# Kernel tuning notes

Measured on AMD Instinct MI355X. Metric: run time of the kernel, lower is better.

The kernel has to match this reference:

```python
import jax, jax.numpy as jnp
import numpy as np

W_BITS = 8       # default precision = max(precisions)
MIN_PREC = 4     # min(precisions)
GROUP_SIZE = 128


def make_new_byte_indices(total_bytes: int) -> np.ndarray:
    # Replicates make_new_byte_indices_torch. Note: in the torch code,
    # argsort(argsort(new_idx)) == new_idx (it is a permutation), so the
    # "unpermute" is a gather with new_idx itself.
    bytes_per_thread = 4
    threads_per_warp = 32
    bytes_per_warp = threads_per_warp * bytes_per_thread  # 128
    full = total_bytes // bytes_per_warp * bytes_per_warp
    rem = total_bytes - full
    parts = []
    if full > 0:
        bi = np.arange(full)
        warp_offsets = (bi // bytes_per_warp) * bytes_per_warp
        thread_indices = bi % threads_per_warp
        byte_off = ((bi % bytes_per_warp) // threads_per_warp) ^ 3
        parts.append(warp_offsets + thread_indices * bytes_per_thread + byte_off)
    if rem > 0:
        ri = np.arange(rem)
        adj = rem // bytes_per_thread
        if adj > 0:
            warp_offsets = (ri // bytes_per_warp) * bytes_per_warp
            thread_indices = ri % adj
            byte_off = (ri // adj) ^ 3
            parts.append(warp_offsets + thread_indices * 4 + byte_off + full)
        else:
            parts.append(np.arange(full, full + rem))
    return np.concatenate(parts).astype(np.int64)


def dequant(qweight, scale, zero, w_bits=W_BITS):
    _, N, in_chunks = qweight.shape
    total_bytes = in_chunks * 4
    in_features = in_chunks * 32
    q = qweight[:w_bits]
    # little-endian byte view of int32 (matches torch .view(torch.uint8))
    b = jnp.stack([(q >> (8 * k)) & 0xFF for k in range(4)], axis=-1)
    b = b.reshape(w_bits, N, total_bytes)  # int32 values in [0,255]
    idx = jnp.asarray(make_new_byte_indices(total_bytes))
    b = b[:, :, idx]
    # unpack bits, MSB first within each byte
    bits = jnp.stack([(b >> i) & 1 for i in reversed(range(8))], axis=-1)
    bits = bits.reshape(w_bits, N, in_features)  # [w_bits, N, in_features]
    plane_w = jnp.asarray([1 << (w_bits - 1 - k) for k in range(w_bits)], dtype=jnp.int32)
    qw = jnp.einsum('b,bni->ni', plane_w, bits)  # int32 in [0, 2^w_bits-1]
    weight_f = qw.astype(jnp.float32)
    bit_err = w_bits - MIN_PREC
    zero = zero * (2.0 ** bit_err)
    scale_pc = jnp.repeat(scale, GROUP_SIZE, axis=1)[:, :in_features]
    zero_pc = jnp.repeat(zero, GROUP_SIZE, axis=1)[:, :in_features]
    return scale_pc * (weight_f - zero_pc)  # [N, in_features]


def setup_inputs() -> dict:
    key = jax.random.key(0)
    kx, kq, ks, kz, kb = jax.random.split(key, 5)
    B, S, IN, OUT, G = 4, 2048, 4096, 4096, GROUP_SIZE
    x = jax.random.normal(kx, (B, S, IN), dtype=jnp.float32)
    qweight = jax.random.randint(kq, (8, OUT, IN // 32), 0, 2147483647, dtype=jnp.int32)
    scale = jax.random.uniform(ks, (OUT, IN // G), dtype=jnp.float32) * 0.01 + 1e-4
    zero = jax.random.uniform(kz, (OUT, IN // G), dtype=jnp.float32) * 8.0
    bias = jax.random.normal(kb, (OUT,), dtype=jnp.float32)
    return {"x": x, "qweight": qweight, "scale": scale, "zero": zero, "bias": bias}


def reference(x, qweight, scale, zero, bias):
    weight = dequant(qweight, scale, zero, W_BITS)  # [out, in]
    return jnp.matmul(x, weight.T) + bias
```

## Files before the change

### kernel.cpp

```cpp
#include <hip/hip_runtime.h>
#include <hip/hip_bf16.h>
#include <stdint.h>

typedef __attribute__((ext_vector_type(8))) short short8;
typedef __attribute__((ext_vector_type(4))) float f32x4;

#define M_DIM 8192
#define N_DIM 4096
#define K_DIM 4096
#define BM 256
#define BN 256
#define BK 64

static __device__ __forceinline__ unsigned short f32_to_bf16(float f) {
  union { float f; unsigned int u; } v; v.f = f;
  unsigned int u = v.u;
  u += 0x7fffu + ((u >> 16) & 1u);
  return (unsigned short)(u >> 16);
}

__global__ void prep_kernel(const float* __restrict__ x,
                            unsigned short* __restrict__ xb,
                            const int* __restrict__ qw,
                            const float* __restrict__ scale,
                            const float* __restrict__ zero,
                            unsigned short* __restrict__ W) {
  if (blockIdx.x < 16384) {
    size_t i = ((size_t)blockIdx.x * blockDim.x + threadIdx.x) * 8;
    float4 v0 = *reinterpret_cast<const float4*>(x + i);
    float4 v1 = *reinterpret_cast<const float4*>(x + i + 4);
    short8 o;
    o[0] = (short)f32_to_bf16(v0.x);
    o[1] = (short)f32_to_bf16(v0.y);
    o[2] = (short)f32_to_bf16(v0.z);
    o[3] = (short)f32_to_bf16(v0.w);
    o[4] = (short)f32_to_bf16(v1.x);
    o[5] = (short)f32_to_bf16(v1.y);
    o[6] = (short)f32_to_bf16(v1.z);
    o[7] = (short)f32_to_bf16(v1.w);
    *reinterpret_cast<short8*>(xb + i) = o;
  } else {
    int idx = (blockIdx.x - 16384) * blockDim.x + threadIdx.x;
    int n = idx >> 7;
    int c = idx & 127;
    unsigned int w[8];
#pragma unroll
    for (int k = 0; k < 8; ++k)
      w[k] = (unsigned int)qw[(size_t)k * (N_DIM * 128) + idx];
    int wp = c >> 5, t = c & 31;
#pragma unroll
    for (int s = 0; s < 4; ++s) {
      int r = s ^ 3;
      unsigned int by[8];
#pragma unroll
      for (int k = 0; k < 8; ++k) by[k] = (w[k] >> (8 * r)) & 0xffu;
      int ibase = wp * 1024 + s * 256 + t * 8;
      int g = ibase >> 7;
      float sc = scale[n * 32 + g];
      float zp = zero[n * 32 + g] * 16.0f;
      short8 o;
#pragma unroll
      for (int u = 0; u < 8; ++u) {
        unsigned int q = 0;
#pragma unroll
        for (int k = 0; k < 8; ++k)
          q |= ((by[k] >> (7 - u)) & 1u) << (7 - k);
        o[u] = (short)f32_to_bf16(sc * ((float)q - zp));
      }
      *reinterpret_cast<short8*>(&W[(size_t)n * K_DIM + ibase]) = o;
    }
  }
}


#define VMCNT2 asm volatile("s_waitcnt vmcnt(2)" ::: "memory")
#define VMCNT0 asm volatile("s_waitcnt vmcnt(0)" ::: "memory")
#define NOOP ((void)0)
#define SB0 __builtin_amdgcn_sched_barrier(0)

#define STG(G, GROWB, KT, LDSC) do {                                           \
  const unsigned short* sb_ = (G) + ((size_t)(GROWB) * K_DIM + (KT) * 64);     \
  __builtin_amdgcn_global_load_lds(                                            \
      (const __attribute__((address_space(1))) void*)(sb_ + s_off0),           \
      (__attribute__((address_space(3))) void*)(smem + (LDSC) + wslot),        \
      16, 0, 0);                                                               \
  __builtin_amdgcn_global_load_lds(                                            \
      (const __attribute__((address_space(1))) void*)(sb_ + s_off1),           \
      (__attribute__((address_space(3))) void*)(smem + (LDSC) + 8192 + wslot), \
      16, 0, 0);                                                               \
} while (0)
#define STG_A(BUF, H, KT) STG(Ag, m0 + (H)*128, (KT), ((BUF)*2 + (H)) * 16384)
#define STG_B(BUF, H, KT) STG(Bg, n0 + (H)*128, (KT), 65536 + ((BUF)*2 + (H)) * 16384)

#define LA(BUF, QM, KK) do {                                                   \
  _Pragma("unroll") for (int mf_ = 0; mf_ < 4; ++mf_)                          \
    a_[mf_][KK] = *(const short8*)(smem + ((KK) ? a_off1 : a_off0) +           \
        (((BUF)*2 + (QM)) * 16384 + mf_ * 2048));                              \
} while (0)
#define LB(BUF, QN, KK) do {                                                   \
  _Pragma("unroll") for (int nf_ = 0; nf_ < 2; ++nf_)                          \
    b_[nf_][KK] = *(const short8*)(smem + ((KK) ? b_off1 : b_off0) +           \
        (((BUF)*2 + (QN)) * 16384 + nf_ * 2048));                              \
} while (0)

#define MFMA_KK(QM, QN, KK)                                                    \
  _Pragma("unroll") for (int mf_ = 0; mf_ < 4; ++mf_)                          \
    _Pragma("unroll") for (int nf_ = 0; nf_ < 2; ++nf_)                        \
      acc[QM][QN][mf_][nf_] = __builtin_amdgcn_mfma_f32_16x16x32_bf16(         \
          a_[mf_][KK], b_[nf_][KK], acc[QM][QN][mf_][nf_], 0, 0, 0)

#define REGION(QM, QN, RD0, RD1, STAGE, WAITV) do {                            \
  __builtin_amdgcn_s_barrier();                                                \
  WAITV;                                                                       \
  SB0;                                                                         \
  __builtin_amdgcn_s_setprio(1);                                               \
  STAGE;                                                                       \
  MFMA_KK(QM, QN, 0);                                                          \
  RD0;                                                                         \
  SB0;                                                                         \
  MFMA_KK(QM, QN, 1);                                                          \
  RD1;                                                                         \
  SB0;                                                                         \
  __builtin_amdgcn_s_setprio(0);                                               \
} while (0)

__global__ __launch_bounds__(512, 2) void gemm_kernel(
    const unsigned short* __restrict__ Ag,
    const unsigned short* __restrict__ Bg,
    const float* __restrict__ bias,
    float* __restrict__ C) {
  __shared__ __align__(16) char smem[131072];

  int bid = blockIdx.x;
  int cpx = gridDim.x >> 3;
  int swz = (bid & 7) * cpx + (bid >> 3);
  int tm = swz >> 4;
  int tn = swz & 15;
  int m0 = tm * BM, n0 = tn * BN;

  int tid = threadIdx.x;
  int lane = tid & 63;
  int wid = tid >> 6;
  int wr = wid >> 2, wc = wid & 3;

  const int xorv = (lane & 7) << 4;
  const int hi4 = (lane >> 4) << 4;
  const int wrbase = wr * 64 + (lane & 15);
  const int wcbase = wc * 32 + (lane & 15);
  const int a_off0 = (wrbase << 7) + (hi4 ^ xorv);
  const int a_off1 = (wrbase << 7) + ((64 | hi4) ^ xorv);
  const int b_off0 = 65536 + (wcbase << 7) + (hi4 ^ xorv);
  const int b_off1 = 65536 + (wcbase << 7) + ((64 | hi4) ^ xorv);
  const int wslot = (tid >> 6) << 10;
  const int s_lr0 = tid >> 3, s_lr1 = 64 + (tid >> 3);
  const int s_off0 = s_lr0 * K_DIM + (((tid & 7) ^ (s_lr0 & 7)) << 3);
  const int s_off1 = s_lr1 * K_DIM + (((tid & 7) ^ (s_lr1 & 7)) << 3);

  short8 a_[4][2], b_[2][2];
  f32x4 acc[2][2][4][2];
#pragma unroll
  for (int i = 0; i < 2; ++i)
#pragma unroll
    for (int j = 0; j < 2; ++j)
#pragma unroll
      for (int mf = 0; mf < 4; ++mf)
#pragma unroll
        for (int nf = 0; nf < 2; ++nf) acc[i][j][mf][nf] = (f32x4){0.f, 0.f, 0.f, 0.f};

  STG_B(0, 0, 0); STG_A(0, 0, 0); STG_B(0, 1, 0); STG_A(0, 1, 0);
  STG_A(1, 0, 1);
  VMCNT2;
  __builtin_amdgcn_s_barrier();
  LA(0, 0, 0); LB(0, 0, 0); LA(0, 0, 1); LB(0, 0, 1);

  for (int t = 0; t < 31; ++t) {
    const int kt1 = 2 * t + 1;
    REGION(0, 0, LB(0,1,0),            LB(0,1,1),            STG_B(1,0,kt1),   VMCNT2);
    REGION(0, 1, LA(0,1,0),            LA(0,1,1),            STG_B(1,1,kt1),   VMCNT2);
    REGION(1, 1, LB(0,0,0),            LB(0,0,1),            STG_A(1,1,kt1),   VMCNT2);
    REGION(1, 0, LA(1,0,0); LB(1,0,0), LA(1,0,1); LB(1,0,1), STG_B(0,0,kt1+1), VMCNT2);
    REGION(0, 0, LB(1,1,0),            LB(1,1,1),            STG_A(0,0,kt1+1), VMCNT2);
    REGION(0, 1, LA(1,1,0),            LA(1,1,1),            STG_B(0,1,kt1+1), VMCNT2);
    REGION(1, 1, LB(1,0,0),            LB(1,0,1),            STG_A(0,1,kt1+1), VMCNT2);
    REGION(1, 0, LA(0,0,0); LB(0,0,0), LA(0,0,1); LB(0,0,1), STG_A(1,0,kt1+2), VMCNT2);
  }
  REGION(0, 0, LB(0,1,0),            LB(0,1,1),            STG_B(1,0,63), VMCNT2);
  REGION(0, 1, LA(0,1,0),            LA(0,1,1),            STG_B(1,1,63), VMCNT2);
  REGION(1, 1, LB(0,0,0),            LB(0,0,1),            STG_A(1,1,63), VMCNT2);
  REGION(1, 0, LA(1,0,0); LB(1,0,0), LA(1,0,1); LB(1,0,1), NOOP,          VMCNT2);
  REGION(0, 0, LB(1,1,0),            LB(1,1,1),            NOOP,          VMCNT0);
  REGION(0, 1, LA(1,1,0),            LA(1,1,1),            NOOP,          NOOP);
  REGION(1, 1, LB(1,0,0),            LB(1,0,1),            NOOP,          NOOP);
  REGION(1, 0, NOOP,                 NOOP,                 NOOP,          NOOP);

#pragma unroll
  for (int qn = 0; qn < 2; ++qn)
#pragma unroll
    for (int nf = 0; nf < 2; ++nf) {
      int gcol = n0 + qn * 128 + wc * 32 + nf * 16 + (lane & 15);
      float bv = bias[gcol];
#pragma unroll
      for (int qm = 0; qm < 2; ++qm)
#pragma unroll
        for (int mf = 0; mf < 4; ++mf) {
          int grow = m0 + qm * 128 + wr * 64 + mf * 16 + ((lane >> 4) << 2);
          f32x4 v = acc[qm][qn][mf][nf];
#pragma unroll
          for (int j = 0; j < 4; ++j)
            C[(size_t)(grow + j) * N_DIM + gcol] = v[j] + bv;
        }
    }
}

extern "C" void kernel_launch(void* const* d_in, const int* in_sizes, int n_in,
                              void* d_out, int out_size, void* d_ws, size_t ws_size,
                              hipStream_t stream) {
  const float* x       = (const float*)d_in[0];
  const int*   qweight = (const int*)d_in[1];
  const float* scale   = (const float*)d_in[2];
  const float* zero    = (const float*)d_in[3];
  const float* bias    = (const float*)d_in[4];
  float* out = (float*)d_out;

  unsigned short* Xb = (unsigned short*)d_ws;
  unsigned short* Wb = Xb + (size_t)M_DIM * K_DIM;

  prep_kernel<<<16384 + 2048, 256, 0, stream>>>(x, Xb, qweight, scale, zero, Wb);
  gemm_kernel<<<(M_DIM / BM) * (N_DIM / BN), 512, 0, stream>>>(Xb, Wb, bias, out);
}
```

Baseline: 260.1 us.

## Fuse fp32-to-bf16 activation conversion into GEMM A-tile staging

```diff
diff --git a/kernel.cpp b/kernel.cpp
--- a/kernel.cpp
+++ b/kernel.cpp
@@ -19,78 +19,78 @@
   return (unsigned short)(u >> 16);
 }
 
-__global__ void prep_kernel(const float* __restrict__ x,
-                            unsigned short* __restrict__ xb,
-                            const int* __restrict__ qw,
+__global__ void prep_kernel(const int* __restrict__ qw,
                             const float* __restrict__ scale,
                             const float* __restrict__ zero,
                             unsigned short* __restrict__ W) {
-  if (blockIdx.x < 16384) {
-    size_t i = ((size_t)blockIdx.x * blockDim.x + threadIdx.x) * 8;
-    float4 v0 = *reinterpret_cast<const float4*>(x + i);
-    float4 v1 = *reinterpret_cast<const float4*>(x + i + 4);
+  int idx = blockIdx.x * blockDim.x + threadIdx.x;
+  int n = idx >> 7;
+  int c = idx & 127;
+  unsigned int w[8];
+#pragma unroll
+  for (int k = 0; k < 8; ++k)
+    w[k] = (unsigned int)qw[(size_t)k * (N_DIM * 128) + idx];
+  int wp = c >> 5, t = c & 31;
+#pragma unroll
+  for (int s = 0; s < 4; ++s) {
+    int r = s ^ 3;
+    unsigned int by[8];
+#pragma unroll
+    for (int k = 0; k < 8; ++k) by[k] = (w[k] >> (8 * r)) & 0xffu;
+    int ibase = wp * 1024 + s * 256 + t * 8;
+    int g = ibase >> 7;
+    float sc = scale[n * 32 + g];
+    float zp = zero[n * 32 + g] * 16.0f;
     short8 o;
-    o[0] = (short)f32_to_bf16(v0.x);
-    o[1] = (short)f32_to_bf16(v0.y);
-    o[2] = (short)f32_to_bf16(v0.z);
-    o[3] = (short)f32_to_bf16(v0.w);
-    o[4] = (short)f32_to_bf16(v1.x);
-    o[5] = (short)f32_to_bf16(v1.y);
-    o[6] = (short)f32_to_bf16(v1.z);
-    o[7] = (short)f32_to_bf16(v1.w);
-    *reinterpret_cast<short8*>(xb + i) = o;
-  } else {
-    int idx = (blockIdx.x - 16384) * blockDim.x + threadIdx.x;
-    int n = idx >> 7;
-    int c = idx & 127;
-    unsigned int w[8];
-#pragma unroll
-    for (int k = 0; k < 8; ++k)
-      w[k] = (unsigned int)qw[(size_t)k * (N_DIM * 128) + idx];
-    int wp = c >> 5, t = c & 31;
-#pragma unroll
-    for (int s = 0; s < 4; ++s) {
-      int r = s ^ 3;
-      unsigned int by[8];
-#pragma unroll
-      for (int k = 0; k < 8; ++k) by[k] = (w[k] >> (8 * r)) & 0xffu;
-      int ibase = wp * 1024 + s * 256 + t * 8;
-      int g = ibase >> 7;
-      float sc = scale[n * 32 + g];
-      float zp = zero[n * 32 + g] * 16.0f;
-      short8 o;
-#pragma unroll
-      for (int u = 0; u < 8; ++u) {
-        unsigned int q = 0;
-#pragma unroll
-        for (int k = 0; k < 8; ++k)
-          q |= ((by[k] >> (7 - u)) & 1u) << (7 - k);
-        o[u] = (short)f32_to_bf16(sc * ((float)q - zp));
-      }
-      *reinterpret_cast<short8*>(&W[(size_t)n * K_DIM + ibase]) = o;
+#pragma unroll
+    for (int u = 0; u < 8; ++u) {
+      unsigned int q = 0;
+#pragma unroll
+      for (int k = 0; k < 8; ++k)
+        q |= ((by[k] >> (7 - u)) & 1u) << (7 - k);
+      o[u] = (short)f32_to_bf16(sc * ((float)q - zp));
     }
+    *reinterpret_cast<short8*>(&W[(size_t)n * K_DIM + ibase]) = o;
   }
 }
 
 
 #define VMCNT2 asm volatile("s_waitcnt vmcnt(2)" ::: "memory")
 #define VMCNT0 asm volatile("s_waitcnt vmcnt(0)" ::: "memory")
+#define LGKM0  asm volatile("s_waitcnt lgkmcnt(0)" ::: "memory")
 #define NOOP ((void)0)
 #define SB0 __builtin_amdgcn_sched_barrier(0)
 
-#define STG(G, GROWB, KT, LDSC) do {                                           \
-  const unsigned short* sb_ = (G) + ((size_t)(GROWB) * K_DIM + (KT) * 64);     \
+#define STG_B(BUF, H, KT) do {                                                 \
+  const unsigned short* sb_ = Bg + ((size_t)(n0 + (H)*128) * K_DIM + (KT) * 64); \
   __builtin_amdgcn_global_load_lds(                                            \
       (const __attribute__((address_space(1))) void*)(sb_ + s_off0),           \
-      (__attribute__((address_space(3))) void*)(smem + (LDSC) + wslot),        \
-      16, 0, 0);                                                               \
+      (__attribute__((address_space(3))) void*)(smem + 65536 +                 \
+          ((BUF)*2 + (H)) * 16384 + wslot), 16, 0, 0);                         \
   __builtin_amdgcn_global_load_lds(                                            \
       (const __attribute__((address_space(1))) void*)(sb_ + s_off1),           \
-      (__attribute__((address_space(3))) void*)(smem + (LDSC) + 8192 + wslot), \
-      16, 0, 0);                                                               \
-} while (0)
-#define STG_A(BUF, H, KT) STG(Ag, m0 + (H)*128, (KT), ((BUF)*2 + (H)) * 16384)
-#define STG_B(BUF, H, KT) STG(Bg, n0 + (H)*128, (KT), 65536 + ((BUF)*2 + (H)) * 16384)
+      (__attribute__((address_space(3))) void*)(smem + 65536 +                 \
+          ((BUF)*2 + (H)) * 16384 + 8192 + wslot), 16, 0, 0);                  \
+} while (0)
+
+#define STG_A(BUF, H, KT) do {                                                 \
+  const float* xs_ = Xf + a_src + ((size_t)(m0 + (H)*128) * K_DIM + (KT)*64);  \
+  float4 f0_ = *(const float4*)(xs_);                                          \
+  float4 f1_ = *(const float4*)(xs_ + 4);                                      \
+  float4 f2_ = *(const float4*)(xs_ + 8);                                      \
+  float4 f3_ = *(const float4*)(xs_ + 12);                                     \
+  short8 w0_, w1_;                                                             \
+  w0_[0] = (short)f32_to_bf16(f0_.x); w0_[1] = (short)f32_to_bf16(f0_.y);      \
+  w0_[2] = (short)f32_to_bf16(f0_.z); w0_[3] = (short)f32_to_bf16(f0_.w);      \
+  w0_[4] = (short)f32_to_bf16(f1_.x); w0_[5] = (short)f32_to_bf16(f1_.y);      \
+  w0_[6] = (short)f32_to_bf16(f1_.z); w0_[7] = (short)f32_to_bf16(f1_.w);      \
+  w1_[0] = (short)f32_to_bf16(f2_.x); w1_[1] = (short)f32_to_bf16(f2_.y);      \
+  w1_[2] = (short)f32_to_bf16(f2_.z); w1_[3] = (short)f32_to_bf16(f2_.w);      \
+  w1_[4] = (short)f32_to_bf16(f3_.x); w1_[5] = (short)f32_to_bf16(f3_.y);      \
+  w1_[6] = (short)f32_to_bf16(f3_.z); w1_[7] = (short)f32_to_bf16(f3_.w);      \
+  *(short8*)(smem + ((BUF)*2 + (H)) * 16384 + aw_off0) = w0_;                  \
+  *(short8*)(smem + ((BUF)*2 + (H)) * 16384 + aw_off1) = w1_;                  \
+} while (0)
 
 #define LA(BUF, QM, KK) do {                                                   \
   _Pragma("unroll") for (int mf_ = 0; mf_ < 4; ++mf_)                          \
@@ -112,6 +112,7 @@
 #define REGION(QM, QN, RD0, RD1, STAGE, WAITV) do {                            \
   __builtin_amdgcn_s_barrier();                                                \
   WAITV;                                                                       \
+  LGKM0;                                                                       \
   SB0;                                                                         \
   __builtin_amdgcn_s_setprio(1);                                               \
   STAGE;                                                                       \
@@ -125,7 +126,7 @@
 } while (0)
 
 __global__ __launch_bounds__(512, 2) void gemm_kernel(
-    const unsigned short* __restrict__ Ag,
+    const float* __restrict__ Xf,
     const unsigned short* __restrict__ Bg,
     const float* __restrict__ bias,
     float* __restrict__ C) {
@@ -151,10 +152,15 @@
   const int a_off1 = (wrbase << 7) + ((64 | hi4) ^ xorv);
   const int b_off0 = 65536 + (wcbase << 7) + (hi4 ^ xorv);
   const int b_off1 = 65536 + (wcbase << 7) + ((64 | hi4) ^ xorv);
-  const int wslot = (tid >> 6) << 10;
+  const int wslot = wid << 10;
   const int s_lr0 = tid >> 3, s_lr1 = 64 + (tid >> 3);
   const int s_off0 = s_lr0 * K_DIM + (((tid & 7) ^ (s_lr0 & 7)) << 3);
   const int s_off1 = s_lr1 * K_DIM + (((tid & 7) ^ (s_lr1 & 7)) << 3);
+  const int aw_row = tid >> 2;
+  const int aq = tid & 3;
+  const size_t a_src = (size_t)aw_row * K_DIM + aq * 16;
+  const int aw_off0 = (aw_row << 7) + (((aq * 2) ^ (aw_row & 7)) << 4);
+  const int aw_off1 = (aw_row << 7) + (((aq * 2 + 1) ^ (aw_row & 7)) << 4);
 
   short8 a_[4][2], b_[2][2];
   f32x4 acc[2][2][4][2];
@@ -169,7 +175,9 @@
 
   STG_B(0, 0, 0); STG_A(0, 0, 0); STG_B(0, 1, 0); STG_A(0, 1, 0);
   STG_A(1, 0, 1);
-  VMCNT2;
+  VMCNT0;
+  LGKM0;
+  SB0;
   __builtin_amdgcn_s_barrier();
   LA(0, 0, 0); LB(0, 0, 0); LA(0, 0, 1); LB(0, 0, 1);
 
@@ -182,7 +190,7 @@
     REGION(0, 0, LB(1,1,0),            LB(1,1,1),            STG_A(0,0,kt1+1), VMCNT2);
     REGION(0, 1, LA(1,1,0),            LA(1,1,1),            STG_B(0,1,kt1+1), VMCNT2);
     REGION(1, 1, LB(1,0,0),            LB(1,0,1),            STG_A(0,1,kt1+1), VMCNT2);
-    REGION(1, 0, LA(0,0,0); LB(0,0,0), LA(0,0,1); LB(0,0,1), STG_A(1,0,kt1+2), VMCNT2);
+    REGION(1, 0, LA(0,0,0); LB(0,0,0), LA(0,0,1); LB(0,0,1), STG_A(1,0,kt1+2), VMCNT0);
   }
   REGION(0, 0, LB(0,1,0),            LB(0,1,1),            STG_B(1,0,63), VMCNT2);
   REGION(0, 1, LA(0,1,0),            LA(0,1,1),            STG_B(1,1,63), VMCNT2);
@@ -222,9 +230,8 @@
   const float* bias    = (const float*)d_in[4];
   float* out = (float*)d_out;
 
-  unsigned short* Xb = (unsigned short*)d_ws;
-  unsigned short* Wb = Xb + (size_t)M_DIM * K_DIM;
-
-  prep_kernel<<<16384 + 2048, 256, 0, stream>>>(x, Xb, qweight, scale, zero, Wb);
-  gemm_kernel<<<(M_DIM / BM) * (N_DIM / BN), 512, 0, stream>>>(Xb, Wb, bias, out);
-}
+  unsigned short* Wb = (unsigned short*)d_ws;
+
+  prep_kernel<<<2048, 256, 0, stream>>>(qweight, scale, zero, Wb);
+  gemm_kernel<<<(M_DIM / BM) * (N_DIM / BN), 512, 0, stream>>>(x, Wb, bias, out);
+}
```

Result: slower. 434.6 us (+67.1%).
